# Kernel optimization log

Measured on AMD Instinct MI355X. Metric: run time of the kernel, lower is better.

Reference implementation:

```python
import jax, jax.numpy as jnp
import numpy as np

N_STATE = 1024
N_HEAD = 16
HEAD_DIM = N_STATE // N_HEAD
SEQLENS = [1024, 896, 768, 640, 512, 384, 896, 1024]  # sum = 6144
TOTAL = sum(SEQLENS)


def setup_inputs() -> dict:
    key = jax.random.key(0)
    ks = jax.random.split(key, 8)
    s = 0.02
    cu = jnp.asarray(np.concatenate([[0], np.cumsum(SEQLENS)]), dtype=jnp.int32)
    return {
        "x": jax.random.normal(ks[0], (TOTAL, N_STATE), jnp.float32),
        "cu_seqlens": cu,
        "Wq": jax.random.normal(ks[1], (N_STATE, N_STATE), jnp.float32) * s,
        "bq": jax.random.normal(ks[2], (N_STATE,), jnp.float32) * s,
        "Wk": jax.random.normal(ks[3], (N_STATE, N_STATE), jnp.float32) * s,
        "Wv": jax.random.normal(ks[4], (N_STATE, N_STATE), jnp.float32) * s,
        "bv": jax.random.normal(ks[5], (N_STATE,), jnp.float32) * s,
        "Wo": jax.random.normal(ks[6], (N_STATE, N_STATE), jnp.float32) * s,
        "bo": jax.random.normal(ks[7], (N_STATE,), jnp.float32) * s,
    }


def reference(x, cu_seqlens, Wq, bq, Wk, Wv, bv, Wo, bo):
    # cu_seqlens is a static (host) quantity in the original (used via .tolist())
    cu = np.asarray(jax.device_get(cu_seqlens))
    seqlens = cu[1:] - cu[:-1]
    B = len(seqlens)
    Lmax = int(seqlens.max())

    q = x @ Wq.T + bq              # [T, n_state]
    k = x @ Wk.T                   # key has no bias
    v = x @ Wv.T + bv

    # static pad/unpad index maps (honoring the ragged structure)
    ar = np.arange(Lmax)
    valid = ar[None, :] < seqlens[:, None]             # [B, Lmax]
    idx = np.where(valid, cu[:-1, None] + ar[None, :], 0)
    unpad_idx = np.nonzero(valid.reshape(-1))[0]       # flat positions of real tokens
    valid_j = jnp.asarray(valid)

    def pad(t):  # [T, n_state] -> [B, Lmax, H, D], zeros in padding
        p = jnp.where(valid_j[:, :, None], t[idx], 0.0)
        return p.reshape(B, Lmax, N_HEAD, HEAD_DIM)

    qp, kp, vp = pad(q), pad(k), pad(v)
    scale = HEAD_DIM ** -0.5
    # torch adds the bool mask (True->1.0) after masked_fill(mask==0, -max):
    # valid keys get +1.0 (softmax-invariant shift), invalid keys get -finfo.max
    big_neg = jnp.finfo(x.dtype).max
    add_mask = jnp.where(valid_j, 1.0, -big_neg)[:, None, None, :]  # [B,1,1,Lmax]

    scores = jnp.einsum("bqhd,bkhd->bhqk", qp, kp) * scale + add_mask
    weights = jax.nn.softmax(scores, axis=-1)
    ctx = jnp.einsum("bhqk,bkhd->bqhd", weights, vp)   # [B, Lmax, H, D]
    ctx_flat = ctx.reshape(B * Lmax, N_STATE)[unpad_idx]  # [T, n_state]
    return ctx_flat @ Wo.T + bo
```

## Files before the change

kernel.cpp:

```cpp
#include <hip/hip_runtime.h>

typedef unsigned short u16;
typedef unsigned int u32;
typedef __attribute__((ext_vector_type(8))) short bf16x8;
typedef __attribute__((ext_vector_type(4))) float f32x4;

#define MFMA_BF16(a, b, c) __builtin_amdgcn_mfma_f32_16x16x32_bf16((a), (b), (c), 0, 0, 0)

#define QSCALE 0.18033688011112042f

__device__ __forceinline__ u16 f2bf(float f) {
    union { float f; unsigned u; } v; v.f = f;
    return (u16)((v.u + 0x7FFFu + ((v.u >> 16) & 1u)) >> 16);
}

__device__ __forceinline__ u32 cvtpk(float a, float b) {
    u32 r;
    asm("v_cvt_pk_bf16_f32 %0, %1, %2" : "=v"(r) : "v"(a), "v"(b));
    return r;
}

__device__ __forceinline__ void async16(const void* g, void* l) {
    __builtin_amdgcn_global_load_lds(
        (const __attribute__((address_space(1))) void*)g,
        (__attribute__((address_space(3))) void*)l, 16, 0, 0);
}

__global__ __launch_bounds__(256) void cvt_all(
    const float* __restrict__ x, const float* __restrict__ Wq, const float* __restrict__ Wk,
    const float* __restrict__ Wv, const float* __restrict__ Wo,
    u16* __restrict__ xb, u16* __restrict__ Wqb, u16* __restrict__ Wkb,
    u16* __restrict__ Wvb, u16* __restrict__ Wob) {
    int b = blockIdx.x;
    const float* src; u16* dst; int base;
    if (b < 6144)      { src = x;  dst = xb;  base = b; }
    else if (b < 7168) { src = Wq; dst = Wqb; base = b - 6144; }
    else if (b < 8192) { src = Wk; dst = Wkb; base = b - 7168; }
    else if (b < 9216) { src = Wv; dst = Wvb; base = b - 8192; }
    else               { src = Wo; dst = Wob; base = b - 9216; }
    int i = base * 256 + threadIdx.x;
    float4 v = ((const float4*)src)[i];
    unsigned long long pk = (unsigned long long)f2bf(v.x)
                          | ((unsigned long long)f2bf(v.y) << 16)
                          | ((unsigned long long)f2bf(v.z) << 32)
                          | ((unsigned long long)f2bf(v.w) << 48);
    *(unsigned long long*)(dst + (size_t)i * 4) = pk;
}

__global__ __launch_bounds__(256) void gemm_qkv(
    const u16* __restrict__ xb,
    const u16* __restrict__ Wqb, const u16* __restrict__ Wkb, const u16* __restrict__ Wvb,
    const float* __restrict__ bq, const float* __restrict__ bv,
    u16* __restrict__ qb, u16* __restrict__ kb, u16* __restrict__ vbT) {
    __shared__ __align__(16) u16 As[2][128 * 64];
    __shared__ __align__(16) u16 Bs[2][128 * 64];
    const int tid = threadIdx.x;

    const int fid = blockIdx.x;
    const int xcd = fid & 7;
    const int slot = fid >> 3;
    const int mloc = slot % 6;
    const int nidx = slot / 6;
    const int m0 = (xcd * 6 + mloc) << 7;
    const int buf = nidx >> 3;
    const int n0 = (nidx & 7) << 7;
    const u16* __restrict__ W = (buf == 0) ? Wqb : (buf == 1) ? Wkb : Wvb;

    const int rr = tid >> 3;
    const int cg = tid & 7;
    const int wv = tid >> 6, lane = tid & 63, g = lane >> 4, c = lane & 15;
    const int wm = (wv & 1) << 6, wn = (wv >> 1) << 6;

    const int sw = (cg ^ (rr & 7)) << 3;
    const u16* gA[4]; const u16* gB[4];
#pragma unroll
    for (int r = 0; r < 4; ++r) {
        gA[r] = xb + (size_t)(m0 + (r << 5) + rr) * 1024 + sw;
        gB[r] = W + (size_t)(n0 + (r << 5) + rr) * 1024 + sw;
    }

    f32x4 zero = {0.f, 0.f, 0.f, 0.f};
    f32x4 acc[4][4];
#pragma unroll
    for (int i = 0; i < 4; ++i)
#pragma unroll
        for (int j = 0; j < 4; ++j) acc[i][j] = zero;

#pragma unroll
    for (int r = 0; r < 4; ++r) {
        async16(gA[r], &As[0][(r << 11) + tid * 8]);
        async16(gB[r], &Bs[0][(r << 11) + tid * 8]);
    }
#pragma unroll
    for (int r = 0; r < 4; ++r) {
        async16(gA[r] + 64, &As[1][(r << 11) + tid * 8]);
        async16(gB[r] + 64, &Bs[1][(r << 11) + tid * 8]);
    }
    asm volatile("s_waitcnt vmcnt(8)" ::: "memory");
    __builtin_amdgcn_s_barrier();
    __builtin_amdgcn_sched_barrier(0);

    for (int kt = 0; kt < 16; ++kt) {
        const int cur = kt & 1;
#pragma unroll
        for (int ks = 0; ks < 2; ++ks) {
            bf16x8 af[4], bb[4];
#pragma unroll
            for (int i = 0; i < 4; ++i) {
                int ra = wm + (i << 4) + c;
                af[i] = *(const bf16x8*)(&As[cur][ra * 64 + ((((ks << 2) + g) ^ (ra & 7)) << 3)]);
                int rb = wn + (i << 4) + c;
                bb[i] = *(const bf16x8*)(&Bs[cur][rb * 64 + ((((ks << 2) + g) ^ (rb & 7)) << 3)]);
            }
#pragma unroll
            for (int i = 0; i < 4; ++i)
#pragma unroll
                for (int j = 0; j < 4; ++j) acc[i][j] = MFMA_BF16(af[i], bb[j], acc[i][j]);
        }
        if (kt == 15) break;
        __builtin_amdgcn_sched_barrier(0);
        __builtin_amdgcn_s_barrier();
        if (kt < 14) {
            const int k0 = (kt + 2) << 6;
#pragma unroll
            for (int r = 0; r < 4; ++r) {
                async16(gA[r] + k0, &As[cur][(r << 11) + tid * 8]);
                async16(gB[r] + k0, &Bs[cur][(r << 11) + tid * 8]);
            }
            asm volatile("s_waitcnt vmcnt(8)" ::: "memory");
        } else {
            asm volatile("s_waitcnt vmcnt(0)" ::: "memory");
        }
        __builtin_amdgcn_s_barrier();
        __builtin_amdgcn_sched_barrier(0);
    }

    if (buf == 0) {
#pragma unroll
        for (int j = 0; j < 4; ++j) {
            int col = n0 + wn + (j << 4) + c;
            float bias = bq[col];
#pragma unroll
            for (int i = 0; i < 4; ++i) {
                int rowb = m0 + wm + (i << 4) + (g << 2);
#pragma unroll
                for (int r = 0; r < 4; ++r)
                    qb[(size_t)(rowb + r) * 1024 + col] = f2bf((acc[i][j][r] + bias) * QSCALE);
            }
        }
    } else if (buf == 1) {
#pragma unroll
        for (int j = 0; j < 4; ++j) {
            int col = n0 + wn + (j << 4) + c;
#pragma unroll
            for (int i = 0; i < 4; ++i) {
                int rowb = m0 + wm + (i << 4) + (g << 2);
#pragma unroll
                for (int r = 0; r < 4; ++r)
                    kb[(size_t)(rowb + r) * 1024 + col] = f2bf(acc[i][j][r]);
            }
        }
    } else {
#pragma unroll
        for (int j = 0; j < 4; ++j) {
            int col = n0 + wn + (j << 4) + c;
            float bias = bv[col];
#pragma unroll
            for (int i = 0; i < 4; ++i) {
                int trow = m0 + wm + (i << 4) + (g << 2);
                unsigned long long pk =
                      (unsigned long long)f2bf(acc[i][j][0] + bias)
                    | ((unsigned long long)f2bf(acc[i][j][1] + bias) << 16)
                    | ((unsigned long long)f2bf(acc[i][j][2] + bias) << 32)
                    | ((unsigned long long)f2bf(acc[i][j][3] + bias) << 48);
                *(unsigned long long*)(vbT + (size_t)col * 6144 + trow) = pk;
            }
        }
    }
}

__global__ __launch_bounds__(256) void gemm_out(
    const u16* __restrict__ ctxb, const u16* __restrict__ Wob,
    const float* __restrict__ bo, float* __restrict__ out) {
    __shared__ __align__(16) u16 As[2][64 * 64];
    __shared__ __align__(16) u16 Bs[2][64 * 64];
    const int tid = threadIdx.x;

    const int fid = blockIdx.x;
    const int xcd = fid & 7;
    const int slot = fid >> 3;
    const int mloc = slot % 12;
    const int nidx = slot / 12;
    const int m0 = (xcd * 12 + mloc) << 6;
    const int n0 = nidx << 6;

    const int rr = tid >> 3, cg = tid & 7;
    const int wv = tid >> 6, lane = tid & 63, g = lane >> 4, c = lane & 15;
    const int wm = (wv & 1) << 5, wn = (wv >> 1) << 5;

    const int sw = (cg ^ (rr & 7)) << 3;
    const u16* gA[2]; const u16* gB[2];
#pragma unroll
    for (int r = 0; r < 2; ++r) {
        gA[r] = ctxb + (size_t)(m0 + (r << 5) + rr) * 1024 + sw;
        gB[r] = Wob + (size_t)(n0 + (r << 5) + rr) * 1024 + sw;
    }

    f32x4 zero = {0.f, 0.f, 0.f, 0.f};
    f32x4 acc[2][2];
#pragma unroll
    for (int i = 0; i < 2; ++i)
#pragma unroll
        for (int j = 0; j < 2; ++j) acc[i][j] = zero;

#pragma unroll
    for (int r = 0; r < 2; ++r) {
        async16(gA[r], &As[0][(r << 11) + tid * 8]);
        async16(gB[r], &Bs[0][(r << 11) + tid * 8]);
    }
#pragma unroll
    for (int r = 0; r < 2; ++r) {
        async16(gA[r] + 64, &As[1][(r << 11) + tid * 8]);
        async16(gB[r] + 64, &Bs[1][(r << 11) + tid * 8]);
    }
    asm volatile("s_waitcnt vmcnt(4)" ::: "memory");
    __builtin_amdgcn_s_barrier();
    __builtin_amdgcn_sched_barrier(0);

    for (int kt = 0; kt < 16; ++kt) {
        const int cur = kt & 1;
#pragma unroll
        for (int ks = 0; ks < 2; ++ks) {
            bf16x8 af[2], bb[2];
#pragma unroll
            for (int i = 0; i < 2; ++i) {
                int ra = wm + (i << 4) + c;
                af[i] = *(const bf16x8*)(&As[cur][ra * 64 + ((((ks << 2) + g) ^ (ra & 7)) << 3)]);
                int rb = wn + (i << 4) + c;
                bb[i] = *(const bf16x8*)(&Bs[cur][rb * 64 + ((((ks << 2) + g) ^ (rb & 7)) << 3)]);
            }
#pragma unroll
            for (int i = 0; i < 2; ++i)
#pragma unroll
                for (int j = 0; j < 2; ++j) acc[i][j] = MFMA_BF16(af[i], bb[j], acc[i][j]);
        }
        if (kt == 15) break;
        __builtin_amdgcn_sched_barrier(0);
        __builtin_amdgcn_s_barrier();
        if (kt < 14) {
            const int k0 = (kt + 2) << 6;
#pragma unroll
            for (int r = 0; r < 2; ++r) {
                async16(gA[r] + k0, &As[cur][(r << 11) + tid * 8]);
                async16(gB[r] + k0, &Bs[cur][(r << 11) + tid * 8]);
            }
            asm volatile("s_waitcnt vmcnt(4)" ::: "memory");
        } else {
            asm volatile("s_waitcnt vmcnt(0)" ::: "memory");
        }
        __builtin_amdgcn_s_barrier();
        __builtin_amdgcn_sched_barrier(0);
    }

#pragma unroll
    for (int j = 0; j < 2; ++j) {
        int col = n0 + wn + (j << 4) + c;
        float bias = bo[col];
#pragma unroll
        for (int i = 0; i < 2; ++i) {
            int rowb = m0 + wm + (i << 4) + (g << 2);
#pragma unroll
            for (int r = 0; r < 4; ++r)
                out[(size_t)(rowb + r) * 1024 + col] = acc[i][j][r] + bias;
        }
    }
}

__global__ __launch_bounds__(256) void attn_kernel(const u16* __restrict__ qb,
                                                   const u16* __restrict__ kb,
                                                   const u16* __restrict__ vbT,
                                                   u16* __restrict__ ctxb) {
    __shared__ __align__(16) u16 Ks[128 * 64];
    __shared__ __align__(16) u16 Vs[64 * 128];
    __shared__ __align__(16) u16 Ps[4 * 2048];

    const int tid = threadIdx.x;
    const int fid = blockIdx.x;
    const int xcd = fid & 7;
    const int slot = fid >> 3;
    const int h = (xcd << 1) + (slot >= 96 ? 1 : 0);
    const int q0 = (slot % 96) << 6;

    const int cuv[9] = {0, 1024, 1920, 2688, 3328, 3840, 4224, 5120, 6144};
    int s0 = 0, e0 = 6144;
#pragma unroll
    for (int i = 1; i < 8; ++i) {
        if (q0 >= cuv[i]) s0 = cuv[i];
        if (q0 < cuv[i] && cuv[i] < e0) e0 = cuv[i];
    }
    const int ntiles = (e0 - s0) >> 7;

    const int wv = tid >> 6, lane = tid & 63, g = lane >> 4, c = lane & 15;
    const int wrow = wv << 4;

    const u16* qp = qb + (size_t)(q0 + wrow + c) * 1024 + (h << 6) + (g << 3);
    bf16x8 qf0 = *(const bf16x8*)(qp);
    bf16x8 qf1 = *(const bf16x8*)(qp + 32);

    float m_run = -1e30f;
    f32x4 zero = {0.f, 0.f, 0.f, 0.f};
    f32x4 oacc[4];
#pragma unroll
    for (int nt = 0; nt < 4; ++nt) oacc[nt] = zero;
    f32x4 lacc = zero;

    const short one_bf = (short)0x3F80;
    const bf16x8 vones = {one_bf, one_bf, one_bf, one_bf,
                          one_bf, one_bf, one_bf, one_bf};

    const int pbase = (wv << 11) + c * 128;
    const int c7 = c & 7;

    for (int kt = 0; kt < ntiles; ++kt) {
        const int kv0 = s0 + (kt << 7);
        __syncthreads();
        {
            const int rr = tid >> 3, cg = tid & 7;
#pragma unroll
            for (int r = 0; r < 4; ++r) {
                int row = (r << 5) + rr;
                async16(kb + (size_t)(kv0 + row) * 1024 + (h << 6) + ((cg ^ (row & 7)) << 3),
                        Ks + (r << 11) + tid * 8);
            }
            const int rr2 = tid >> 4, cg2 = tid & 15;
#pragma unroll
            for (int r = 0; r < 4; ++r) {
                int row = (r << 4) + rr2;
                async16(vbT + (size_t)((h << 6) + row) * 6144 + kv0 + ((cg2 ^ (row & 15)) << 3),
                        Vs + (r << 11) + tid * 8);
            }
        }
        __syncthreads();

        f32x4 st[8];
#pragma unroll
        for (int mt = 0; mt < 8; ++mt) st[mt] = zero;
        __builtin_amdgcn_s_setprio(1);
#pragma unroll
        for (int mt = 0; mt < 8; ++mt) {
            int row = (mt << 4) + c;
            int sw = row & 7;
            bf16x8 kf0 = *(const bf16x8*)(&Ks[row * 64 + ((g ^ sw) << 3)]);
            bf16x8 kf1 = *(const bf16x8*)(&Ks[row * 64 + (((4 + g) ^ sw) << 3)]);
            st[mt] = MFMA_BF16(kf0, qf0, st[mt]);
            st[mt] = MFMA_BF16(kf1, qf1, st[mt]);
        }
        __builtin_amdgcn_s_setprio(0);

        float mx = fmaxf(fmaxf(st[0][0], st[0][1]), fmaxf(st[0][2], st[0][3]));
#pragma unroll
        for (int mt = 1; mt < 8; ++mt) {
            float a = fmaxf(st[mt][0], fmaxf(st[mt][1], st[mt][2]));
            mx = fmaxf(mx, fmaxf(a, st[mt][3]));
        }
        mx = fmaxf(mx, __shfl_xor(mx, 16, 64));
        mx = fmaxf(mx, __shfl_xor(mx, 32, 64));

        if (!__all(mx - m_run <= 8.f)) {
            float mnew = fmaxf(m_run, mx);
            float alpha = exp2f(m_run - mnew);
            m_run = mnew;
            float al[4];
#pragma unroll
            for (int r = 0; r < 4; ++r) al[r] = __shfl(alpha, (g << 2) + r, 16);
#pragma unroll
            for (int nt = 0; nt < 4; ++nt)
#pragma unroll
                for (int r = 0; r < 4; ++r) oacc[nt][r] *= al[r];
#pragma unroll
            for (int r = 0; r < 4; ++r) lacc[r] *= al[r];
        }

#pragma unroll
        for (int mt = 0; mt < 8; ++mt) {
            float p0 = exp2f(st[mt][0] - m_run);
            float p1 = exp2f(st[mt][1] - m_run);
            float p2 = exp2f(st[mt][2] - m_run);
            float p3 = exp2f(st[mt][3] - m_run);
            int ph = ((mt << 2) + g) ^ (c7 << 1);
            *(uint2*)(Ps + pbase + (ph << 2)) = make_uint2(cvtpk(p0, p1), cvtpk(p2, p3));
        }

        __builtin_amdgcn_s_setprio(1);
#pragma unroll
        for (int ks = 0; ks < 4; ++ks) {
            int pg = ((ks << 2) + g) ^ c7;
            bf16x8 pf = *(const bf16x8*)(Ps + pbase + (pg << 3));
            lacc = MFMA_BF16(pf, vones, lacc);
#pragma unroll
            for (int nt = 0; nt < 4; ++nt) {
                int vrow = (nt << 4) + c;
                bf16x8 vf = *(const bf16x8*)(&Vs[vrow * 128 + ((((ks << 2) + g) ^ (vrow & 15)) << 3)]);
                oacc[nt] = MFMA_BF16(pf, vf, oacc[nt]);
            }
        }
        __builtin_amdgcn_s_setprio(0);
    }

    float invr[4];
#pragma unroll
    for (int r = 0; r < 4; ++r) invr[r] = 1.0f / lacc[r];
#pragma unroll
    for (int r = 0; r < 4; ++r) {
        size_t rowoff = (size_t)(q0 + wrow + (g << 2) + r) * 1024 + (h << 6);
#pragma unroll
        for (int nt = 0; nt < 4; ++nt)
            ctxb[rowoff + (nt << 4) + c] = f2bf(oacc[nt][r] * invr[r]);
    }
}

extern "C" void kernel_launch(void* const* d_in, const int* in_sizes, int n_in,
                              void* d_out, int out_size, void* d_ws, size_t ws_size,
                              hipStream_t stream) {
    const float* x  = (const float*)d_in[0];
    const float* Wq = (const float*)d_in[2];
    const float* bq = (const float*)d_in[3];
    const float* Wk = (const float*)d_in[4];
    const float* Wv = (const float*)d_in[5];
    const float* bv = (const float*)d_in[6];
    const float* Wo = (const float*)d_in[7];
    const float* bo = (const float*)d_in[8];
    float* out = (float*)d_out;

    u16* ws = (u16*)d_ws;
    u16* xb   = ws;
    u16* Wqb  = xb + 6291456;
    u16* Wkb  = Wqb + 1048576;
    u16* Wvb  = Wkb + 1048576;
    u16* Wob  = Wvb + 1048576;
    u16* qb   = Wob + 1048576;
    u16* kb   = qb + 6291456;
    u16* vbT  = kb + 6291456;
    u16* ctxb = xb;

    cvt_all<<<10240, 256, 0, stream>>>(x, Wq, Wk, Wv, Wo, xb, Wqb, Wkb, Wvb, Wob);
    gemm_qkv<<<1152, 256, 0, stream>>>(xb, Wqb, Wkb, Wvb, bq, bv, qb, kb, vbT);
    attn_kernel<<<1536, 256, 0, stream>>>(qb, kb, vbT, ctxb);
    gemm_out<<<1536, 256, 0, stream>>>(ctxb, Wob, bo, out);
}
```

Baseline: 227.0 us.

## Switch QKV GEMM to triple-buffered 32-wide K tiles with new swizzle

```diff
diff --git a/kernel.cpp b/kernel.cpp
--- a/kernel.cpp
+++ b/kernel.cpp
@@ -52,8 +52,8 @@
     const u16* __restrict__ Wqb, const u16* __restrict__ Wkb, const u16* __restrict__ Wvb,
     const float* __restrict__ bq, const float* __restrict__ bv,
     u16* __restrict__ qb, u16* __restrict__ kb, u16* __restrict__ vbT) {
-    __shared__ __align__(16) u16 As[2][128 * 64];
-    __shared__ __align__(16) u16 Bs[2][128 * 64];
+    __shared__ __align__(16) u16 As[3][4096];
+    __shared__ __align__(16) u16 Bs[3][4096];
     const int tid = threadIdx.x;
 
     const int fid = blockIdx.x;
@@ -66,17 +66,17 @@
     const int n0 = (nidx & 7) << 7;
     const u16* __restrict__ W = (buf == 0) ? Wqb : (buf == 1) ? Wkb : Wvb;
 
-    const int rr = tid >> 3;
-    const int cg = tid & 7;
     const int wv = tid >> 6, lane = tid & 63, g = lane >> 4, c = lane & 15;
     const int wm = (wv & 1) << 6, wn = (wv >> 1) << 6;
 
-    const int sw = (cg ^ (rr & 7)) << 3;
-    const u16* gA[4]; const u16* gB[4];
-#pragma unroll
-    for (int r = 0; r < 4; ++r) {
-        gA[r] = xb + (size_t)(m0 + (r << 5) + rr) * 1024 + sw;
-        gB[r] = W + (size_t)(n0 + (r << 5) + rr) * 1024 + sw;
+    const int gg = (tid & 7) ^ ((tid >> 3) & 7);
+    const int half = gg >> 2, kg = gg & 3;
+    const int grow = ((tid >> 3) << 1) + half;
+    const u16* srcA[2]; const u16* srcB[2];
+#pragma unroll
+    for (int r = 0; r < 2; ++r) {
+        srcA[r] = xb + (size_t)(m0 + (r << 6) + grow) * 1024 + (kg << 3);
+        srcB[r] = W + (size_t)(n0 + (r << 6) + grow) * 1024 + (kg << 3);
     }
 
     f32x4 zero = {0.f, 0.f, 0.f, 0.f};
@@ -86,53 +86,53 @@
 #pragma unroll
         for (int j = 0; j < 4; ++j) acc[i][j] = zero;
 
-#pragma unroll
-    for (int r = 0; r < 4; ++r) {
-        async16(gA[r], &As[0][(r << 11) + tid * 8]);
-        async16(gB[r], &Bs[0][(r << 11) + tid * 8]);
-    }
-#pragma unroll
-    for (int r = 0; r < 4; ++r) {
-        async16(gA[r] + 64, &As[1][(r << 11) + tid * 8]);
-        async16(gB[r] + 64, &Bs[1][(r << 11) + tid * 8]);
-    }
+    const int sgo = (((((c & 1) << 2) | g) ^ (c >> 1)) << 3);
+    const int r2a = (wm >> 1) + (c >> 1);
+    const int r2b = (wn >> 1) + (c >> 1);
+
+    auto stage = [&](int tile, int b) {
+        const int k0 = tile << 5;
+#pragma unroll
+        for (int r = 0; r < 2; ++r) {
+            async16(srcA[r] + k0, &As[b][(r << 11) + tid * 8]);
+            async16(srcB[r] + k0, &Bs[b][(r << 11) + tid * 8]);
+        }
+    };
+
+    stage(0, 0);
+    stage(1, 1);
+    stage(2, 2);
     asm volatile("s_waitcnt vmcnt(8)" ::: "memory");
     __builtin_amdgcn_s_barrier();
     __builtin_amdgcn_sched_barrier(0);
 
-    for (int kt = 0; kt < 16; ++kt) {
-        const int cur = kt & 1;
-#pragma unroll
-        for (int ks = 0; ks < 2; ++ks) {
-            bf16x8 af[4], bb[4];
-#pragma unroll
-            for (int i = 0; i < 4; ++i) {
-                int ra = wm + (i << 4) + c;
-                af[i] = *(const bf16x8*)(&As[cur][ra * 64 + ((((ks << 2) + g) ^ (ra & 7)) << 3)]);
-                int rb = wn + (i << 4) + c;
-                bb[i] = *(const bf16x8*)(&Bs[cur][rb * 64 + ((((ks << 2) + g) ^ (rb & 7)) << 3)]);
-            }
-#pragma unroll
-            for (int i = 0; i < 4; ++i)
-#pragma unroll
-                for (int j = 0; j < 4; ++j) acc[i][j] = MFMA_BF16(af[i], bb[j], acc[i][j]);
-        }
-        if (kt == 15) break;
+    int b = 0;
+    for (int kt = 0; kt < 32; ++kt) {
+        bf16x8 af[4], bb[4];
+#pragma unroll
+        for (int i = 0; i < 4; ++i) {
+            af[i] = *(const bf16x8*)(&As[b][((r2a + (i << 3)) << 6) + sgo]);
+            bb[i] = *(const bf16x8*)(&Bs[b][((r2b + (i << 3)) << 6) + sgo]);
+        }
+#pragma unroll
+        for (int i = 0; i < 4; ++i)
+#pragma unroll
+            for (int j = 0; j < 4; ++j) acc[i][j] = MFMA_BF16(af[i], bb[j], acc[i][j]);
+
+        if (kt == 31) break;
         __builtin_amdgcn_sched_barrier(0);
         __builtin_amdgcn_s_barrier();
-        if (kt < 14) {
-            const int k0 = (kt + 2) << 6;
-#pragma unroll
-            for (int r = 0; r < 4; ++r) {
-                async16(gA[r] + k0, &As[cur][(r << 11) + tid * 8]);
-                async16(gB[r] + k0, &Bs[cur][(r << 11) + tid * 8]);
-            }
+        if (kt < 29) {
+            stage(kt + 3, b);
             asm volatile("s_waitcnt vmcnt(8)" ::: "memory");
+        } else if (kt == 29) {
+            asm volatile("s_waitcnt vmcnt(4)" ::: "memory");
         } else {
             asm volatile("s_waitcnt vmcnt(0)" ::: "memory");
         }
         __builtin_amdgcn_s_barrier();
         __builtin_amdgcn_sched_barrier(0);
+        b = (b == 2) ? 0 : b + 1;
     }
 
     if (buf == 0) {
```

Measured after the change: 232.1 us. +2.3%, slower.
